# Performance work log

Measured on AMD Instinct MI355X. Metric: run time of the kernel, lower is better.

The kernel has to match this reference:

```python
import jax, jax.numpy as jnp
import numpy as np

B, S, HID = 4, 2048, 1024
NH, HD = 16, 64  # op_heads, head_size (hidden_size // total_heads)
EPS = 1e-6


def setup_inputs() -> dict:
    key = jax.random.key(0)
    k1, k2, k3, k4 = jax.random.split(key, 4)
    return {
        "hidden_states": jax.random.normal(k1, (B, S, HID), dtype=jnp.float32),
        "assoc_hc_attn": jax.random.uniform(k2, (B, S, S), dtype=jnp.float32),
        "broad_hc_attn": jax.random.uniform(k3, (B, S, S), dtype=jnp.float32),
        "Wv": jax.random.normal(k4, (HID, NH * HD), dtype=jnp.float32) * 0.02,
        "bv": jnp.zeros((NH * HD,), dtype=jnp.float32),
    }


def reference(hidden_states, assoc_hc_attn, broad_hc_attn, Wv, bv):
    # v_proj + split heads -> [B, NH, S, HD]
    value = hidden_states @ Wv + bv
    sp_value = value.reshape(B, S, NH, HD).transpose(0, 2, 1, 3)

    # broad_heads == 0, so attn_heads == assoc_hc_attn broadcast over all op_heads.
    attn = assoc_hc_attn.astype(jnp.float32)  # [B, S, S]
    causal = jnp.tril(jnp.ones((S, S), dtype=bool))
    attn = jnp.where(causal, attn, 0.0)
    # sum-normalize along keys (no softmax)
    attn = attn / (EPS + attn.sum(axis=-1, keepdims=True))

    # shared attn across heads: contract once -> [B, NH, S, HD]
    out = jnp.einsum('bqk,bhkd->bhqd', attn, sp_value)
    # merge heads -> [B, S, NH*HD]
    return out.transpose(0, 2, 1, 3).reshape(B, S, NH * HD)
```

## Files before the change

kernel.cpp:

```cpp
#include <hip/hip_runtime.h>

#define B_    4
#define S_    2048
#define HID_  1024
#define NO_   1024
#define EPS_  1e-6f
#define M1_   (B_ * S_)

typedef __attribute__((ext_vector_type(8))) short  short8;
typedef __attribute__((ext_vector_type(4))) float  f32x4;
typedef unsigned short ushort_t;

__device__ __forceinline__ unsigned short f2bf(float f) {
  union { float f; unsigned int u; } v; v.f = f;
  unsigned int r = v.u + 0x7FFFu + ((v.u >> 16) & 1u);
  return (unsigned short)(r >> 16);
}
__device__ __forceinline__ unsigned pack2(float a, float b) {
  return (unsigned)f2bf(a) | ((unsigned)f2bf(b) << 16);
}

typedef __attribute__((address_space(1))) const void GASV;
typedef __attribute__((address_space(3))) void LASV;
__device__ __forceinline__ void gld16(const void* g, void* l) {
  __builtin_amdgcn_global_load_lds((GASV*)g, (LASV*)l, 16, 0, 0);
}

__global__ __launch_bounds__(256) void k_prep(
    const float* __restrict__ Wv, ushort_t* __restrict__ WvT,
    const float* __restrict__ H,  ushort_t* __restrict__ Hb,
    const float* __restrict__ A,  ushort_t* __restrict__ Ab) {
  int id = blockIdx.x;
  if (id < 1024) {
    __shared__ float tile[32][33];
    int k0 = (id & 31) * 32;
    int n0 = (id >> 5) * 32;
    int tx = threadIdx.x & 31, ty = threadIdx.x >> 5;
    for (int i = ty; i < 32; i += 8)
      tile[i][tx] = Wv[(size_t)(k0 + i) * NO_ + n0 + tx];
    __syncthreads();
    for (int i = ty; i < 32; i += 8)
      WvT[(size_t)(n0 + i) * HID_ + k0 + tx] = f2bf(tile[tx][i]);
  } else if (id < 1024 + 8192) {
    size_t i = ((size_t)(id - 1024) * 256 + threadIdx.x) * 4;
    float4 v = *(const float4*)(H + i);
    uint2 p; p.x = pack2(v.x, v.y); p.y = pack2(v.z, v.w);
    *(uint2*)(Hb + i) = p;
  } else {
    int row  = (id - 9216) * 4 + (threadIdx.x >> 6);
    int lane = threadIdx.x & 63;
    int q = row & 2047;
    int wend = ((q >> 7) + 1) << 7;
    const float* rp = A + (size_t)row * S_;
    float4 v[8];
    float s = 0.f;
#pragma unroll
    for (int i = 0; i < 8; i++) {
      int k = i * 256 + lane * 4;
      if (k < wend) {
        float4 t = *(const float4*)(rp + k);
        t.x = (k + 0 <= q) ? t.x : 0.f;
        t.y = (k + 1 <= q) ? t.y : 0.f;
        t.z = (k + 2 <= q) ? t.z : 0.f;
        t.w = (k + 3 <= q) ? t.w : 0.f;
        v[i] = t;
        s += t.x + t.y + t.z + t.w;
      }
    }
    for (int off = 1; off < 64; off <<= 1) s += __shfl_xor(s, off, 64);
    float inv = 1.0f / (EPS_ + s);
    ushort_t* op = Ab + (size_t)row * S_;
#pragma unroll
    for (int i = 0; i < 8; i++) {
      int k = i * 256 + lane * 4;
      if (k < wend) {
        uint2 p;
        p.x = pack2(v[i].x * inv, v[i].y * inv);
        p.y = pack2(v[i].z * inv, v[i].w * inv);
        *(uint2*)(op + k) = p;
      }
    }
  }
}

__global__ __launch_bounds__(512) void k_vt(
    const ushort_t* __restrict__ WvT, const ushort_t* __restrict__ Hb,
    const float* __restrict__ bv, ushort_t* __restrict__ Vt) {
  __shared__ __align__(16) char lds[3 * 32768];
  int id  = blockIdx.x;
  int xcd = id & 7;
  int mem = id >> 3;
  int n0  = (mem & 7) * 128;
  int m0  = (xcd * 8 + (mem >> 3)) * 128;
  int tid = threadIdx.x;
  int wave = tid >> 6, lane = tid & 63;
  int lq = lane >> 4, lm = lane & 15;
  int wq = wave >> 2, wn = wave & 3;

  int rr = lane >> 2;
  int sc = (lane & 3) ^ ((rr >> 1) & 3);
  int fo = (lq ^ ((lm >> 1) & 3)) << 4;
  const ushort_t* pa = WvT + (size_t)(n0 + wave * 16 + rr) * HID_ + sc * 8;
  const ushort_t* pb = Hb  + (size_t)(m0 + wave * 16 + rr) * HID_ + sc * 8;

  f32x4 acc[4][2];
  for (int i = 0; i < 4; i++) for (int j = 0; j < 2; j++) acc[i][j] = (f32x4)0.0f;

  const int N = 16;

#pragma unroll
  for (int tpre = 0; tpre < 2; ++tpre) {
    char* wb = lds + tpre * 32768;
    gld16(pa,      wb + wave * 1024);
    gld16(pa + 32, wb + 8192  + wave * 1024);
    gld16(pb,      wb + 16384 + wave * 1024);
    gld16(pb + 32, wb + 24576 + wave * 1024);
    pa += 64; pb += 64;
  }
  asm volatile("s_waitcnt vmcnt(4)" ::: "memory");
  __builtin_amdgcn_s_barrier();

  int rbuf = 0;
  for (int it = 0; it < N; ++it) {
    int wbuf = rbuf + 2; if (wbuf >= 3) wbuf -= 3;
    bool stg = (it + 2) < N;
    const char* ra = lds + rbuf * 32768;
    char* wb = lds + wbuf * 32768;
    short8 af[4], bf0, bf1;
#pragma unroll
    for (int mi = 0; mi < 4; mi++)
      af[mi] = *(const short8*)(ra + (wq * 64 + mi * 16 + lm) * 64 + fo);
    bf0 = *(const short8*)(ra + 16384 + (wn * 32 +  0 + lm) * 64 + fo);
    bf1 = *(const short8*)(ra + 16384 + (wn * 32 + 16 + lm) * 64 + fo);
    if (stg) { gld16(pa, wb + wave * 1024); gld16(pb, wb + 16384 + wave * 1024); }
    __builtin_amdgcn_s_barrier();
    __builtin_amdgcn_s_setprio(1);
#pragma unroll
    for (int mi = 0; mi < 4; mi++) {
      acc[mi][0] = __builtin_amdgcn_mfma_f32_16x16x32_bf16(af[mi], bf0, acc[mi][0], 0, 0, 0);
      acc[mi][1] = __builtin_amdgcn_mfma_f32_16x16x32_bf16(af[mi], bf1, acc[mi][1], 0, 0, 0);
    }
    __builtin_amdgcn_s_setprio(0);
    __builtin_amdgcn_s_barrier();
#pragma unroll
    for (int mi = 0; mi < 4; mi++)
      af[mi] = *(const short8*)(ra + 8192 + (wq * 64 + mi * 16 + lm) * 64 + fo);
    bf0 = *(const short8*)(ra + 24576 + (wn * 32 +  0 + lm) * 64 + fo);
    bf1 = *(const short8*)(ra + 24576 + (wn * 32 + 16 + lm) * 64 + fo);
    if (stg) { gld16(pa + 32, wb + 8192 + wave * 1024); gld16(pb + 32, wb + 24576 + wave * 1024); pa += 64; pb += 64; }
    __builtin_amdgcn_s_barrier();
    __builtin_amdgcn_s_setprio(1);
#pragma unroll
    for (int mi = 0; mi < 4; mi++) {
      acc[mi][0] = __builtin_amdgcn_mfma_f32_16x16x32_bf16(af[mi], bf0, acc[mi][0], 0, 0, 0);
      acc[mi][1] = __builtin_amdgcn_mfma_f32_16x16x32_bf16(af[mi], bf1, acc[mi][1], 0, 0, 0);
    }
    __builtin_amdgcn_s_setprio(0);
    if (it < N - 1) {
      if (it + 2 < N) asm volatile("s_waitcnt vmcnt(4)" ::: "memory");
      else            asm volatile("s_waitcnt vmcnt(0)" ::: "memory");
    }
    __builtin_amdgcn_s_barrier();
    rbuf = (rbuf == 2) ? 0 : rbuf + 1;
  }
  for (int mi = 0; mi < 4; mi++) {
    for (int r = 0; r < 4; r++) {
      int n = n0 + wq * 64 + mi * 16 + lq * 4 + r;
      float bias = bv[n];
      for (int ni = 0; ni < 2; ni++) {
        int m = m0 + wn * 32 + ni * 16 + lm;
        int b = m >> 11;
        int s = m & 2047;
        Vt[((size_t)b * NO_ + n) * S_ + s] = f2bf(acc[mi][ni][r] + bias);
      }
    }
  }
}

__global__ __launch_bounds__(512) void k_attn(
    const ushort_t* __restrict__ Ab, const ushort_t* __restrict__ Vt,
    float* __restrict__ out) {
  __shared__ __align__(16) char lds[3 * 32768];
  int id  = blockIdx.x;
  int xcd = id & 7;
  int mem = id >> 3;
  int b   = xcd >> 1;
  int n0  = ((xcd & 1) * 4 + (mem & 3)) * 128;
  int y   = mem >> 2;
  int tid = threadIdx.x;
  int wave = tid >> 6, lane = tid & 63;
  int lq = lane >> 4, lm = lane & 15;
  int wq = wave >> 2, wn = wave & 3;

  int rr = lane >> 2;
  int sc = (lane & 3) ^ ((rr >> 1) & 3);
  int fo = (lq ^ ((lm >> 1) & 3)) << 4;
  const ushort_t* pb0 = Vt + (size_t)(b * NO_ + n0 + wave * 16 + rr) * S_ + sc * 8;

  for (int seg = 0; seg < 2; ++seg) {
    int t  = seg ? (15 - y) : y;
    int q0 = t * 128;
    const int N = 2 * (t + 1);
    const ushort_t* pa = Ab + (size_t)(b * S_ + q0 + wave * 16 + rr) * S_ + sc * 8;
    const ushort_t* pb = pb0;

    f32x4 acc[4][2];
    for (int i = 0; i < 4; i++) for (int j = 0; j < 2; j++) acc[i][j] = (f32x4)0.0f;

#pragma unroll
    for (int tpre = 0; tpre < 2; ++tpre) {
      char* wb = lds + tpre * 32768;
      gld16(pa,      wb + wave * 1024);
      gld16(pa + 32, wb + 8192  + wave * 1024);
      gld16(pb,      wb + 16384 + wave * 1024);
      gld16(pb + 32, wb + 24576 + wave * 1024);
      pa += 64; pb += 64;
    }
    asm volatile("s_waitcnt vmcnt(4)" ::: "memory");
    __builtin_amdgcn_s_barrier();

    int rbuf = 0;
    for (int it = 0; it < N; ++it) {
      int wbuf = rbuf + 2; if (wbuf >= 3) wbuf -= 3;
      bool stg = (it + 2) < N;
      const char* ra = lds + rbuf * 32768;
      char* wb = lds + wbuf * 32768;
      short8 af[4], bf0, bf1;
#pragma unroll
      for (int mi = 0; mi < 4; mi++)
        af[mi] = *(const short8*)(ra + (wq * 64 + mi * 16 + lm) * 64 + fo);
      bf0 = *(const short8*)(ra + 16384 + (wn * 32 +  0 + lm) * 64 + fo);
      bf1 = *(const short8*)(ra + 16384 + (wn * 32 + 16 + lm) * 64 + fo);
      if (stg) { gld16(pa, wb + wave * 1024); gld16(pb, wb + 16384 + wave * 1024); }
      __builtin_amdgcn_s_barrier();
      __builtin_amdgcn_s_setprio(1);
#pragma unroll
      for (int mi = 0; mi < 4; mi++) {
        acc[mi][0] = __builtin_amdgcn_mfma_f32_16x16x32_bf16(af[mi], bf0, acc[mi][0], 0, 0, 0);
        acc[mi][1] = __builtin_amdgcn_mfma_f32_16x16x32_bf16(af[mi], bf1, acc[mi][1], 0, 0, 0);
      }
      __builtin_amdgcn_s_setprio(0);
      __builtin_amdgcn_s_barrier();
#pragma unroll
      for (int mi = 0; mi < 4; mi++)
        af[mi] = *(const short8*)(ra + 8192 + (wq * 64 + mi * 16 + lm) * 64 + fo);
      bf0 = *(const short8*)(ra + 24576 + (wn * 32 +  0 + lm) * 64 + fo);
      bf1 = *(const short8*)(ra + 24576 + (wn * 32 + 16 + lm) * 64 + fo);
      if (stg) { gld16(pa + 32, wb + 8192 + wave * 1024); gld16(pb + 32, wb + 24576 + wave * 1024); pa += 64; pb += 64; }
      __builtin_amdgcn_s_barrier();
      __builtin_amdgcn_s_setprio(1);
#pragma unroll
      for (int mi = 0; mi < 4; mi++) {
        acc[mi][0] = __builtin_amdgcn_mfma_f32_16x16x32_bf16(af[mi], bf0, acc[mi][0], 0, 0, 0);
        acc[mi][1] = __builtin_amdgcn_mfma_f32_16x16x32_bf16(af[mi], bf1, acc[mi][1], 0, 0, 0);
      }
      __builtin_amdgcn_s_setprio(0);
      if (it < N - 1) {
        if (it + 2 < N) asm volatile("s_waitcnt vmcnt(4)" ::: "memory");
        else            asm volatile("s_waitcnt vmcnt(0)" ::: "memory");
      }
      __builtin_amdgcn_s_barrier();
      rbuf = (rbuf == 2) ? 0 : rbuf + 1;
    }
    for (int mi = 0; mi < 4; mi++) {
      for (int r = 0; r < 4; r++) {
        int q = q0 + wq * 64 + mi * 16 + lq * 4 + r;
        for (int ni = 0; ni < 2; ni++) {
          int n = n0 + wn * 32 + ni * 16 + lm;
          out[((size_t)(b * S_ + q)) * NO_ + n] = acc[mi][ni][r];
        }
      }
    }
    asm volatile("s_waitcnt vmcnt(0)" ::: "memory");
    __builtin_amdgcn_s_barrier();
  }
}

extern "C" void kernel_launch(void* const* d_in, const int* in_sizes, int n_in,
                              void* d_out, int out_size, void* d_ws, size_t ws_size,
                              hipStream_t stream) {
  const float* H  = (const float*)d_in[0];
  const float* A  = (const float*)d_in[1];
  const float* Wv = (const float*)d_in[3];
  const float* bv = (const float*)d_in[4];
  float* out = (float*)d_out;

  char* ws = (char*)d_ws;
  ushort_t* WvT = (ushort_t*)ws;
  ushort_t* Hb  = (ushort_t*)(ws + 2097152);
  ushort_t* Vt  = (ushort_t*)(ws + 2097152 + 16777216);
  ushort_t* Abf = (ushort_t*)(ws + 2097152 + 2 * 16777216);

  k_prep <<<1024 + 8192 + 2048, 256, 0, stream>>>(Wv, WvT, H, Hb, A, Abf);
  k_vt   <<<512, 512, 0, stream>>>(WvT, Hb, bv, Vt);
  k_attn <<<256, 512, 0, stream>>>(Abf, Vt, out);
}
```

Baseline: 214.3 us.

## Co-schedule attention normalization with V projection and use 256-thread 128x128 tiles

```diff
diff --git a/kernel.cpp b/kernel.cpp
--- a/kernel.cpp
+++ b/kernel.cpp
@@ -26,10 +26,9 @@
   __builtin_amdgcn_global_load_lds((GASV*)g, (LASV*)l, 16, 0, 0);
 }
 
-__global__ __launch_bounds__(256) void k_prep(
+__global__ __launch_bounds__(256) void k_prep0(
     const float* __restrict__ Wv, ushort_t* __restrict__ WvT,
-    const float* __restrict__ H,  ushort_t* __restrict__ Hb,
-    const float* __restrict__ A,  ushort_t* __restrict__ Ab) {
+    const float* __restrict__ H,  ushort_t* __restrict__ Hb) {
   int id = blockIdx.x;
   if (id < 1024) {
     __shared__ float tile[32][33];
@@ -41,13 +40,106 @@
     __syncthreads();
     for (int i = ty; i < 32; i += 8)
       WvT[(size_t)(n0 + i) * HID_ + k0 + tx] = f2bf(tile[tx][i]);
-  } else if (id < 1024 + 8192) {
+  } else {
     size_t i = ((size_t)(id - 1024) * 256 + threadIdx.x) * 4;
     float4 v = *(const float4*)(H + i);
     uint2 p; p.x = pack2(v.x, v.y); p.y = pack2(v.z, v.w);
     *(uint2*)(Hb + i) = p;
+  }
+}
+
+__global__ __launch_bounds__(256, 3) void k_vtA(
+    const ushort_t* __restrict__ WvT, const ushort_t* __restrict__ Hb,
+    const float* __restrict__ bv, ushort_t* __restrict__ Vt,
+    const float* __restrict__ A, ushort_t* __restrict__ Ab) {
+  __shared__ __align__(16) char lds[3 * 16384];
+  int id = blockIdx.x;
+  if (id < 512) {
+    int xcd = id & 7;
+    int mem = id >> 3;
+    int n0  = (mem & 7) * 128;
+    int m0  = (xcd * 8 + (mem >> 3)) * 128;
+    int tid = threadIdx.x;
+    int wave = tid >> 6, lane = tid & 63;
+    int lq = lane >> 4, lm = lane & 15;
+    int wq = wave >> 1, wm = wave & 1;
+
+    int rr = lane >> 2;
+    int sc = (lane & 3) ^ ((rr >> 1) & 3);
+    int fo = (lq ^ ((lm >> 1) & 3)) << 4;
+    const ushort_t* pa = WvT + (size_t)(n0 + wave * 32 + rr) * HID_ + sc * 8;
+    const ushort_t* pb = Hb  + (size_t)(m0 + wave * 32 + rr) * HID_ + sc * 8;
+
+    f32x4 acc[4][4];
+    for (int i = 0; i < 4; i++) for (int j = 0; j < 4; j++) acc[i][j] = (f32x4)0.0f;
+
+    const int N = 32;
+#pragma unroll
+    for (int tpre = 0; tpre < 2; ++tpre) {
+      char* wb = lds + tpre * 16384;
+      gld16(pa,             wb + wave * 2048);
+      gld16(pa + 16 * HID_, wb + wave * 2048 + 1024);
+      gld16(pb,             wb + 8192 + wave * 2048);
+      gld16(pb + 16 * HID_, wb + 8192 + wave * 2048 + 1024);
+      pa += 32; pb += 32;
+    }
+    asm volatile("s_waitcnt vmcnt(4)" ::: "memory");
+    __builtin_amdgcn_s_barrier();
+
+    int rbuf = 0;
+    for (int it = 0; it < N; ++it) {
+      int wbuf = rbuf + 2; if (wbuf >= 3) wbuf -= 3;
+      bool stg = (it + 2) < N;
+      const char* ra = lds + rbuf * 16384;
+      char* wb = lds + wbuf * 16384;
+      short8 af[4], bf0, bf1;
+#pragma unroll
+      for (int mi = 0; mi < 4; mi++)
+        af[mi] = *(const short8*)(ra + (wq * 64 + mi * 16 + lm) * 64 + fo);
+      bf0 = *(const short8*)(ra + 8192 + (wm * 64 +  0 + lm) * 64 + fo);
+      bf1 = *(const short8*)(ra + 8192 + (wm * 64 + 16 + lm) * 64 + fo);
+      if (stg) { gld16(pb, wb + 8192 + wave * 2048); gld16(pb + 16 * HID_, wb + 8192 + wave * 2048 + 1024); }
+      __builtin_amdgcn_s_barrier();
+      __builtin_amdgcn_s_setprio(1);
+#pragma unroll
+      for (int mi = 0; mi < 4; mi++) {
+        acc[mi][0] = __builtin_amdgcn_mfma_f32_16x16x32_bf16(af[mi], bf0, acc[mi][0], 0, 0, 0);
+        acc[mi][1] = __builtin_amdgcn_mfma_f32_16x16x32_bf16(af[mi], bf1, acc[mi][1], 0, 0, 0);
+      }
+      __builtin_amdgcn_s_setprio(0);
+      __builtin_amdgcn_s_barrier();
+      bf0 = *(const short8*)(ra + 8192 + (wm * 64 + 32 + lm) * 64 + fo);
+      bf1 = *(const short8*)(ra + 8192 + (wm * 64 + 48 + lm) * 64 + fo);
+      if (stg) { gld16(pa, wb + wave * 2048); gld16(pa + 16 * HID_, wb + wave * 2048 + 1024); pa += 32; pb += 32; }
+      __builtin_amdgcn_s_barrier();
+      __builtin_amdgcn_s_setprio(1);
+#pragma unroll
+      for (int mi = 0; mi < 4; mi++) {
+        acc[mi][2] = __builtin_amdgcn_mfma_f32_16x16x32_bf16(af[mi], bf0, acc[mi][2], 0, 0, 0);
+        acc[mi][3] = __builtin_amdgcn_mfma_f32_16x16x32_bf16(af[mi], bf1, acc[mi][3], 0, 0, 0);
+      }
+      __builtin_amdgcn_s_setprio(0);
+      if (it < N - 1) {
+        if (it + 2 < N) asm volatile("s_waitcnt vmcnt(4)" ::: "memory");
+        else            asm volatile("s_waitcnt vmcnt(0)" ::: "memory");
+      }
+      __builtin_amdgcn_s_barrier();
+      rbuf = (rbuf == 2) ? 0 : rbuf + 1;
+    }
+    for (int mi = 0; mi < 4; mi++) {
+      for (int r = 0; r < 4; r++) {
+        int n = n0 + wq * 64 + mi * 16 + lq * 4 + r;
+        float bias = bv[n];
+        for (int ni = 0; ni < 4; ni++) {
+          int m = m0 + wm * 64 + ni * 16 + lm;
+          int b = m >> 11;
+          int s = m & 2047;
+          Vt[((size_t)b * NO_ + n) * S_ + s] = f2bf(acc[mi][ni][r] + bias);
+        }
+      }
+    }
   } else {
-    int row  = (id - 9216) * 4 + (threadIdx.x >> 6);
+    int row  = (id - 512) * 4 + (threadIdx.x >> 6);
     int lane = threadIdx.x & 63;
     int q = row & 2047;
     int wend = ((q >> 7) + 1) << 7;
@@ -83,39 +175,42 @@
   }
 }
 
-__global__ __launch_bounds__(512) void k_vt(
-    const ushort_t* __restrict__ WvT, const ushort_t* __restrict__ Hb,
-    const float* __restrict__ bv, ushort_t* __restrict__ Vt) {
-  __shared__ __align__(16) char lds[3 * 32768];
+__global__ __launch_bounds__(256, 2) void k_attn(
+    const ushort_t* __restrict__ Ab, const ushort_t* __restrict__ Vt,
+    float* __restrict__ out) {
+  __shared__ __align__(16) char lds[3 * 16384];
   int id  = blockIdx.x;
-  int xcd = id & 7;
-  int mem = id >> 3;
-  int n0  = (mem & 7) * 128;
-  int m0  = (xcd * 8 + (mem >> 3)) * 128;
+  int c   = id & 255;
+  int rnd = id >> 8;
+  int col = c & 31;
+  int g   = c >> 5;
+  int t   = rnd ? g : (15 - g);
+  int n0  = (col & 7) * 128;
+  int b   = col >> 3;
+  int q0  = t * 128;
   int tid = threadIdx.x;
   int wave = tid >> 6, lane = tid & 63;
   int lq = lane >> 4, lm = lane & 15;
-  int wq = wave >> 2, wn = wave & 3;
+  int wq = wave >> 1, wn = wave & 1;
 
   int rr = lane >> 2;
   int sc = (lane & 3) ^ ((rr >> 1) & 3);
   int fo = (lq ^ ((lm >> 1) & 3)) << 4;
-  const ushort_t* pa = WvT + (size_t)(n0 + wave * 16 + rr) * HID_ + sc * 8;
-  const ushort_t* pb = Hb  + (size_t)(m0 + wave * 16 + rr) * HID_ + sc * 8;
-
-  f32x4 acc[4][2];
-  for (int i = 0; i < 4; i++) for (int j = 0; j < 2; j++) acc[i][j] = (f32x4)0.0f;
-
-  const int N = 16;
-
+  const ushort_t* pa = Ab + (size_t)(b * S_ + q0 + wave * 32 + rr) * S_ + sc * 8;
+  const ushort_t* pb = Vt + (size_t)(b * NO_ + n0 + wave * 32 + rr) * S_ + sc * 8;
+
+  f32x4 acc[4][4];
+  for (int i = 0; i < 4; i++) for (int j = 0; j < 4; j++) acc[i][j] = (f32x4)0.0f;
+
+  const int N = 4 * t + 4;
 #pragma unroll
   for (int tpre = 0; tpre < 2; ++tpre) {
-    char* wb = lds + tpre * 32768;
-    gld16(pa,      wb + wave * 1024);
-    gld16(pa + 32, wb + 8192  + wave * 1024);
-    gld16(pb,      wb + 16384 + wave * 1024);
-    gld16(pb + 32, wb + 24576 + wave * 1024);
-    pa += 64; pb += 64;
+    char* wb = lds + tpre * 16384;
+    gld16(pa,           wb + wave * 2048);
+    gld16(pa + 16 * S_, wb + wave * 2048 + 1024);
+    gld16(pb,           wb + 8192 + wave * 2048);
+    gld16(pb + 16 * S_, wb + 8192 + wave * 2048 + 1024);
+    pa += 32; pb += 32;
   }
   asm volatile("s_waitcnt vmcnt(4)" ::: "memory");
   __builtin_amdgcn_s_barrier();
@@ -124,15 +219,15 @@
   for (int it = 0; it < N; ++it) {
     int wbuf = rbuf + 2; if (wbuf >= 3) wbuf -= 3;
     bool stg = (it + 2) < N;
-    const char* ra = lds + rbuf * 32768;
-    char* wb = lds + wbuf * 32768;
+    const char* ra = lds + rbuf * 16384;
+    char* wb = lds + wbuf * 16384;
     short8 af[4], bf0, bf1;
 #pragma unroll
     for (int mi = 0; mi < 4; mi++)
       af[mi] = *(const short8*)(ra + (wq * 64 + mi * 16 + lm) * 64 + fo);
-    bf0 = *(const short8*)(ra + 16384 + (wn * 32 +  0 + lm) * 64 + fo);
-    bf1 = *(const short8*)(ra + 16384 + (wn * 32 + 16 + lm) * 64 + fo);
-    if (stg) { gld16(pa, wb + wave * 1024); gld16(pb, wb + 16384 + wave * 1024); }
+    bf0 = *(const short8*)(ra + 8192 + (wn * 64 +  0 + lm) * 64 + fo);
+    bf1 = *(const short8*)(ra + 8192 + (wn * 64 + 16 + lm) * 64 + fo);
+    if (stg) { gld16(pb, wb + 8192 + wave * 2048); gld16(pb + 16 * S_, wb + 8192 + wave * 2048 + 1024); }
     __builtin_amdgcn_s_barrier();
     __builtin_amdgcn_s_setprio(1);
 #pragma unroll
@@ -142,18 +237,15 @@
     }
     __builtin_amdgcn_s_setprio(0);
     __builtin_amdgcn_s_barrier();
-#pragma unroll
-    for (int mi = 0; mi < 4; mi++)
-      af[mi] = *(const short8*)(ra + 8192 + (wq * 64 + mi * 16 + lm) * 64 + fo);
-    bf0 = *(const short8*)(ra + 24576 + (wn * 32 +  0 + lm) * 64 + fo);
-    bf1 = *(const short8*)(ra + 24576 + (wn * 32 + 16 + lm) * 64 + fo);
-    if (stg) { gld16(pa + 32, wb + 8192 + wave * 1024); gld16(pb + 32, wb + 24576 + wave * 1024); pa += 64; pb += 64; }
+    bf0 = *(const short8*)(ra + 8192 + (wn * 64 + 32 + lm) * 64 + fo);
+    bf1 = *(const short8*)(ra + 8192 + (wn * 64 + 48 + lm) * 64 + fo);
+    if (stg) { gld16(pa, wb + wave * 2048); gld16(pa + 16 * S_, wb + wave * 2048 + 1024); pa += 32; pb += 32; }
     __builtin_amdgcn_s_barrier();
     __builtin_amdgcn_s_setprio(1);
 #pragma unroll
     for (int mi = 0; mi < 4; mi++) {
-      acc[mi][0] = __builtin_amdgcn_mfma_f32_16x16x32_bf16(af[mi], bf0, acc[mi][0], 0, 0, 0);
-      acc[mi][1] = __builtin_amdgcn_mfma_f32_16x16x32_bf16(af[mi], bf1, acc[mi][1], 0, 0, 0);
+      acc[mi][2] = __builtin_amdgcn_mfma_f32_16x16x32_bf16(af[mi], bf0, acc[mi][2], 0, 0, 0);
+      acc[mi][3] = __builtin_amdgcn_mfma_f32_16x16x32_bf16(af[mi], bf1, acc[mi][3], 0, 0, 0);
     }
     __builtin_amdgcn_s_setprio(0);
     if (it < N - 1) {
@@ -165,114 +257,12 @@
   }
   for (int mi = 0; mi < 4; mi++) {
     for (int r = 0; r < 4; r++) {
-      int n = n0 + wq * 64 + mi * 16 + lq * 4 + r;
-      float bias = bv[n];
-      for (int ni = 0; ni < 2; ni++) {
-        int m = m0 + wn * 32 + ni * 16 + lm;
-        int b = m >> 11;
-        int s = m & 2047;
-        Vt[((size_t)b * NO_ + n) * S_ + s] = f2bf(acc[mi][ni][r] + bias);
-      }
-    }
-  }
-}
-
-__global__ __launch_bounds__(512) void k_attn(
-    const ushort_t* __restrict__ Ab, const ushort_t* __restrict__ Vt,
-    float* __restrict__ out) {
-  __shared__ __align__(16) char lds[3 * 32768];
-  int id  = blockIdx.x;
-  int xcd = id & 7;
-  int mem = id >> 3;
-  int b   = xcd >> 1;
-  int n0  = ((xcd & 1) * 4 + (mem & 3)) * 128;
-  int y   = mem >> 2;
-  int tid = threadIdx.x;
-  int wave = tid >> 6, lane = tid & 63;
-  int lq = lane >> 4, lm = lane & 15;
-  int wq = wave >> 2, wn = wave & 3;
-
-  int rr = lane >> 2;
-  int sc = (lane & 3) ^ ((rr >> 1) & 3);
-  int fo = (lq ^ ((lm >> 1) & 3)) << 4;
-  const ushort_t* pb0 = Vt + (size_t)(b * NO_ + n0 + wave * 16 + rr) * S_ + sc * 8;
-
-  for (int seg = 0; seg < 2; ++seg) {
-    int t  = seg ? (15 - y) : y;
-    int q0 = t * 128;
-    const int N = 2 * (t + 1);
-    const ushort_t* pa = Ab + (size_t)(b * S_ + q0 + wave * 16 + rr) * S_ + sc * 8;
-    const ushort_t* pb = pb0;
-
-    f32x4 acc[4][2];
-    for (int i = 0; i < 4; i++) for (int j = 0; j < 2; j++) acc[i][j] = (f32x4)0.0f;
-
-#pragma unroll
-    for (int tpre = 0; tpre < 2; ++tpre) {
-      char* wb = lds + tpre * 32768;
-      gld16(pa,      wb + wave * 1024);
-      gld16(pa + 32, wb + 8192  + wave * 1024);
-      gld16(pb,      wb + 16384 + wave * 1024);
-      gld16(pb + 32, wb + 24576 + wave * 1024);
-      pa += 64; pb += 64;
-    }
-    asm volatile("s_waitcnt vmcnt(4)" ::: "memory");
-    __builtin_amdgcn_s_barrier();
-
-    int rbuf = 0;
-    for (int it = 0; it < N; ++it) {
-      int wbuf = rbuf + 2; if (wbuf >= 3) wbuf -= 3;
-      bool stg = (it + 2) < N;
-      const char* ra = lds + rbuf * 32768;
-      char* wb = lds + wbuf * 32768;
-      short8 af[4], bf0, bf1;
-#pragma unroll
-      for (int mi = 0; mi < 4; mi++)
-        af[mi] = *(const short8*)(ra + (wq * 64 + mi * 16 + lm) * 64 + fo);
-      bf0 = *(const short8*)(ra + 16384 + (wn * 32 +  0 + lm) * 64 + fo);
-      bf1 = *(const short8*)(ra + 16384 + (wn * 32 + 16 + lm) * 64 + fo);
-      if (stg) { gld16(pa, wb + wave * 1024); gld16(pb, wb + 16384 + wave * 1024); }
-      __builtin_amdgcn_s_barrier();
-      __builtin_amdgcn_s_setprio(1);
-#pragma unroll
-      for (int mi = 0; mi < 4; mi++) {
-        acc[mi][0] = __builtin_amdgcn_mfma_f32_16x16x32_bf16(af[mi], bf0, acc[mi][0], 0, 0, 0);
-        acc[mi][1] = __builtin_amdgcn_mfma_f32_16x16x32_bf16(af[mi], bf1, acc[mi][1], 0, 0, 0);
-      }
-      __builtin_amdgcn_s_setprio(0);
-      __builtin_amdgcn_s_barrier();
-#pragma unroll
-      for (int mi = 0; mi < 4; mi++)
-        af[mi] = *(const short8*)(ra + 8192 + (wq * 64 + mi * 16 + lm) * 64 + fo);
-      bf0 = *(const short8*)(ra + 24576 + (wn * 32 +  0 + lm) * 64 + fo);
-      bf1 = *(const short8*)(ra + 24576 + (wn * 32 + 16 + lm) * 64 + fo);
-      if (stg) { gld16(pa + 32, wb + 8192 + wave * 1024); gld16(pb + 32, wb + 24576 + wave * 1024); pa += 64; pb += 64; }
-      __builtin_amdgcn_s_barrier();
-      __builtin_amdgcn_s_setprio(1);
-#pragma unroll
-      for (int mi = 0; mi < 4; mi++) {
-        acc[mi][0] = __builtin_amdgcn_mfma_f32_16x16x32_bf16(af[mi], bf0, acc[mi][0], 0, 0, 0);
-        acc[mi][1] = __builtin_amdgcn_mfma_f32_16x16x32_bf16(af[mi], bf1, acc[mi][1], 0, 0, 0);
-      }
-      __builtin_amdgcn_s_setprio(0);
-      if (it < N - 1) {
-        if (it + 2 < N) asm volatile("s_waitcnt vmcnt(4)" ::: "memory");
-        else            asm volatile("s_waitcnt vmcnt(0)" ::: "memory");
-      }
-      __builtin_amdgcn_s_barrier();
-      rbuf = (rbuf == 2) ? 0 : rbuf + 1;
-    }
-    for (int mi = 0; mi < 4; mi++) {
-      for (int r = 0; r < 4; r++) {
-        int q = q0 + wq * 64 + mi * 16 + lq * 4 + r;
-        for (int ni = 0; ni < 2; ni++) {
-          int n = n0 + wn * 32 + ni * 16 + lm;
-          out[((size_t)(b * S_ + q)) * NO_ + n] = acc[mi][ni][r];
-        }
-      }
-    }
-    asm volatile("s_waitcnt vmcnt(0)" ::: "memory");
-    __builtin_amdgcn_s_barrier();
+      int q = q0 + wq * 64 + mi * 16 + lq * 4 + r;
+      for (int ni = 0; ni < 4; ni++) {
+        int n = n0 + wn * 64 + ni * 16 + lm;
+        out[((size_t)(b * S_ + q)) * NO_ + n] = acc[mi][ni][r];
+      }
+    }
   }
 }
 
@@ -291,7 +281,7 @@
   ushort_t* Vt  = (ushort_t*)(ws + 2097152 + 16777216);
   ushort_t* Abf = (ushort_t*)(ws + 2097152 + 2 * 16777216);
 
-  k_prep <<<1024 + 8192 + 2048, 256, 0, stream>>>(Wv, WvT, H, Hb, A, Abf);
-  k_vt   <<<512, 512, 0, stream>>>(WvT, Hb, bv, Vt);
-  k_attn <<<256, 512, 0, stream>>>(Abf, Vt, out);
-}
+  k_prep0<<<1024 + 8192, 256, 0, stream>>>(Wv, WvT, H, Hb);
+  k_vtA  <<<512 + 2048, 256, 0, stream>>>(WvT, Hb, bv, Vt, A, Abf);
+  k_attn <<<512, 256, 0, stream>>>(Abf, Vt, out);
+}
```

Measured after the change: 218.2 us. No clear change (+1.8%).
